# Kernel optimization log

Measured on AMD Instinct MI355X. Metric: run time of the kernel, lower is better.

The kernel has to match this reference:

```python
import jax, jax.numpy as jnp
import numpy as np

NUM_EXPERTS = 8
CAPACITY = 320  # per-batch per-expert token capacity


def setup_inputs() -> dict:
    key = jax.random.key(0)
    k0, k1, k2, k3 = jax.random.split(key, 4)
    B, S, D, F = 4, 2048, 1024, 4096
    E = NUM_EXPERTS
    hidden_states = jax.random.normal(k0, (B, S, D), dtype=jnp.float32)
    gate_w = jax.random.normal(k1, (E, D), dtype=jnp.float32) * 0.02
    w1 = jax.random.normal(k2, (E, D, F), dtype=jnp.float32) * 0.02
    w2 = jax.random.normal(k3, (E, F, D), dtype=jnp.float32) * 0.02
    return {"hidden_states": hidden_states, "gate_w": gate_w, "w1": w1, "w2": w2}


def reference(hidden_states, gate_w, w1, w2):
    E, C = NUM_EXPERTS, CAPACITY
    B, S, D = hidden_states.shape

    # --- route ---
    router_logits = jnp.einsum('bsd,ed->bse', hidden_states, gate_w)
    router_probs = jax.nn.softmax(router_logits, axis=-1)
    expert_idx = jnp.argmax(router_probs, axis=-1)                      # [B,S]
    onehot = jax.nn.one_hot(expert_idx, E, dtype=jnp.int32)             # [B,S,E]
    priority = jnp.cumsum(onehot, axis=1)                               # [B,S,E]
    router_mask = onehot * (priority <= C)                              # [B,S,E]
    assigned = jnp.sum(router_mask, axis=-1) > 0                        # [B,S]
    # slot within expert buffer; dropped tokens go to overflow slot C
    slot = jnp.where(assigned, jnp.sum(priority * onehot, axis=-1) - 1, C)  # [B,S]
    top_prob = jnp.max(router_probs, axis=-1, keepdims=True)            # [B,S,1]

    # --- dispatch: scatter tokens into [B,E,C+1,D] buffers ---
    def dispatch(x_b, e_b, s_b):
        return jnp.zeros((E, C + 1, D), x_b.dtype).at[e_b, s_b].set(x_b)
    buf = jax.vmap(dispatch)(hidden_states, expert_idx, slot)           # [B,E,C+1,D]

    # --- per-expert FFN as grouped GEMM ---
    h = jax.nn.silu(jnp.einsum('becd,edf->becf', buf, w1))
    y = jnp.einsum('becf,efd->becd', h, w2)                             # [B,E,C+1,D]

    # --- combine: gather expert outputs back to token order ---
    gathered = jax.vmap(lambda y_b, e_b, s_b: y_b[e_b, s_b])(y, expert_idx, slot)  # [B,S,D]
    next_states = jnp.where(assigned[..., None], gathered, hidden_states)
    out = top_prob * next_states

    # argmax of capacity-masked one-hot: dropped tokens -> expert 0
    expert_index = jnp.where(assigned, expert_idx, 0)
    return out, router_logits, expert_index
```

## Files before the change

### kernel.cpp

```cpp
#include <hip/hip_runtime.h>

#define B_  4
#define S_  2048
#define D_  1024
#define F_  4096
#define E_  8
#define C_  320
#define CP_ 384
#define NT_ (B_*S_)
#define G_  (B_*E_)

typedef short bf16x8 __attribute__((ext_vector_type(8)));
typedef float f32x4  __attribute__((ext_vector_type(4)));

using gptr_t = const __attribute__((address_space(1))) void*;
using lptr_t = __attribute__((address_space(3))) void*;

__device__ static inline void gll16(const void* g, void* l) {
    __builtin_amdgcn_global_load_lds((gptr_t)g, (lptr_t)l, 16, 0, 0);
}

__device__ static inline unsigned short f2b(float f) {
    unsigned int u = __float_as_uint(f);
    u += 0x7fffu + ((u >> 16) & 1u);
    return (unsigned short)(u >> 16);
}

__global__ __launch_bounds__(256) void k_convT(const float* __restrict__ in,
                                               unsigned short* __restrict__ out,
                                               int R, int Cc) {
    __shared__ unsigned short ld[64][66];
    int e = blockIdx.z;
    const float* src = in + (size_t)e * R * Cc;
    unsigned short* dst = out + (size_t)e * R * Cc;
    int c0 = blockIdx.x * 64, r0 = blockIdx.y * 64;
    int t = threadIdx.x;

    int rr = t >> 4;
    int cg = t & 15;
#pragma unroll
    for (int p = 0; p < 4; p++) {
        int row = p * 16 + rr;
        float4 v = *(const float4*)(src + (size_t)(r0 + row) * Cc + c0 + cg * 4);
        ld[cg * 4 + 0][row] = f2b(v.x);
        ld[cg * 4 + 1][row] = f2b(v.y);
        ld[cg * 4 + 2][row] = f2b(v.z);
        ld[cg * 4 + 3][row] = f2b(v.w);
    }
    __syncthreads();

    int cc = t >> 3;
    int rg = t & 7;
#pragma unroll
    for (int p = 0; p < 2; p++) {
        int col = p * 32 + cc;
        const unsigned* lp = (const unsigned*)&ld[col][rg * 8];
        uint4 w;
        w.x = lp[0]; w.y = lp[1]; w.z = lp[2]; w.w = lp[3];
        *(uint4*)(dst + (size_t)(c0 + col) * R + r0 + rg * 8) = w;
    }
}

__global__ __launch_bounds__(256) void k_router(const float* __restrict__ hs,
                                                const float* __restrict__ gw,
                                                float* __restrict__ logits,
                                                int* __restrict__ eidx,
                                                float* __restrict__ tp) {
    int tok  = (int)((blockIdx.x * 256 + threadIdx.x) >> 6);
    int lane = threadIdx.x & 63;
    const float* x = hs + (size_t)tok * D_;
    double acc[E_];
#pragma unroll
    for (int e = 0; e < E_; e++) acc[e] = 0.0;
    for (int i = 0; i < 16; i++) {
        float xv = x[lane + 64 * i];
#pragma unroll
        for (int e = 0; e < E_; e++)
            acc[e] += (double)xv * (double)gw[e * D_ + lane + 64 * i];
    }
#pragma unroll
    for (int e = 0; e < E_; e++) {
#pragma unroll
        for (int off = 32; off > 0; off >>= 1)
            acc[e] += __shfl_xor(acc[e], off, 64);
    }
    if (lane == 0) {
        float l[E_];
        float mx = -1e30f; int am = 0;
#pragma unroll
        for (int e = 0; e < E_; e++) {
            l[e] = (float)acc[e];
            if (l[e] > mx) { mx = l[e]; am = e; }
        }
        float se = 0.f;
#pragma unroll
        for (int e = 0; e < E_; e++) se += __expf(l[e] - mx);
        tp[tok]   = 1.0f / se;
        eidx[tok] = am;
#pragma unroll
        for (int e = 0; e < E_; e++) logits[(size_t)tok * E_ + e] = l[e];
    }
}

__global__ __launch_bounds__(256) void k_scan(const int* __restrict__ eidx,
                                              int* __restrict__ slot,
                                              int* __restrict__ tok_list,
                                              int* __restrict__ counts,
                                              float* __restrict__ eif) {
    int b = blockIdx.x;
    __shared__ int cCnt[32][E_];
    __shared__ int cBase[32][E_];
    int t = threadIdx.x, wv = t >> 6, lane = t & 63;
    const int* eb = eidx + b * S_;
    for (int c = wv; c < 32; c += 4) {
        int e = eb[c * 64 + lane];
#pragma unroll
        for (int x = 0; x < E_; x++) {
            unsigned long long m = __ballot(e == x);
            if (lane == 0) cCnt[c][x] = __popcll(m);
        }
    }
    __syncthreads();
    if (t < E_) {
        int s = 0;
        for (int c = 0; c < 32; c++) { cBase[c][t] = s; s += cCnt[c][t]; }
        counts[b * E_ + t] = s;
    }
    __syncthreads();
    for (int c = wv; c < 32; c += 4) {
        int s_tok = c * 64 + lane;
        int e = eb[s_tok];
        unsigned long long lowmask = (1ull << lane) - 1ull;
        int rank = 0;
#pragma unroll
        for (int x = 0; x < E_; x++) {
            unsigned long long m = __ballot(e == x);
            if (x == e) rank = __popcll(m & lowmask);
        }
        int pos = cBase[c][e] + rank;
        int assigned = (pos < C_);
        slot[b * S_ + s_tok] = assigned ? pos : C_;
        if (assigned) tok_list[(b * E_ + e) * C_ + pos] = s_tok;
        eif[b * S_ + s_tok] = assigned ? (float)e : 0.0f;
    }
}

__global__ __launch_bounds__(256) void k_dispatch(const float* __restrict__ hs,
                                                  const int* __restrict__ tok_list,
                                                  const int* __restrict__ counts,
                                                  unsigned short* __restrict__ Xd) {
    int w    = (int)((blockIdx.x * 256 + threadIdx.x) >> 6);
    int lane = threadIdx.x & 63;
    int g = w / CP_, row = w % CP_;
    int b = g >> 3;
    int n = min(counts[g], C_);
    unsigned short* drow = Xd + ((size_t)g * CP_ + row) * D_;
    if (row < n) {
        int ts = tok_list[g * C_ + row];
        const float* src = hs + ((size_t)b * S_ + ts) * D_;
#pragma unroll
        for (int i = 0; i < 2; i++) {
            int c0 = (lane + 64 * i) * 8;
            float4 v0 = *(const float4*)(src + c0);
            float4 v1 = *(const float4*)(src + c0 + 4);
            uint4 pk;
            pk.x = (unsigned)f2b(v0.x) | ((unsigned)f2b(v0.y) << 16);
            pk.y = (unsigned)f2b(v0.z) | ((unsigned)f2b(v0.w) << 16);
            pk.z = (unsigned)f2b(v1.x) | ((unsigned)f2b(v1.y) << 16);
            pk.w = (unsigned)f2b(v1.z) | ((unsigned)f2b(v1.w) << 16);
            *(uint4*)(drow + c0) = pk;
        }
    } else {
        uint4 z = {0u, 0u, 0u, 0u};
#pragma unroll
        for (int i = 0; i < 2; i++)
            *(uint4*)(drow + (lane + 64 * i) * 8) = z;
    }
}

__global__ __launch_bounds__(256) void k_ffn1(const unsigned short* __restrict__ Xd,
                                              const unsigned short* __restrict__ w1t,
                                              const int* __restrict__ counts,
                                              unsigned short* __restrict__ h) {
    int zz = blockIdx.z;
    int g = (zz & 3) * 8 + (zz >> 2);
    int n_tok = min(counts[g], C_);
    int m0 = blockIdx.y * 128;
    if (m0 >= n_tok) return;
    int n0 = blockIdx.x * 128;
    int e = g & 7;

    __shared__ unsigned short As[128 * 32];
    __shared__ unsigned short Bs[128 * 32];
    int t = threadIdx.x, lane = t & 63, wv = t >> 6, wm = wv >> 1, wn = wv & 1;

    const unsigned short* Ap = Xd  + (size_t)g * CP_ * D_ + (size_t)(m0 + (t >> 2)) * D_ + (t & 3) * 8;
    const unsigned short* Bp = w1t + (size_t)e * F_ * D_  + (size_t)(n0 + (t >> 2)) * D_ + (t & 3) * 8;

    f32x4 acc[4][4];
    f32x4 z = {0.f, 0.f, 0.f, 0.f};
#pragma unroll
    for (int i = 0; i < 4; i++)
#pragma unroll
        for (int j = 0; j < 4; j++) acc[i][j] = z;

    int ar = (wm * 64 + (lane & 15)) * 32 + (lane >> 4) * 8;
    int br = (wn * 64 + (lane & 15)) * 32 + (lane >> 4) * 8;

    for (int kt = 0; kt < D_; kt += 32) {
        __syncthreads();
        gll16(Ap,            (char*)As + wv * 1024);
        gll16(Ap + 64 * D_,  (char*)As + 4096 + wv * 1024);
        gll16(Bp,            (char*)Bs + wv * 1024);
        gll16(Bp + 64 * D_,  (char*)Bs + 4096 + wv * 1024);
        Ap += 32; Bp += 32;
        __syncthreads();
        bf16x8 a[4], bq[4];
#pragma unroll
        for (int i = 0; i < 4; i++) a[i]  = *(const bf16x8*)&As[ar + i * 512];
#pragma unroll
        for (int j = 0; j < 4; j++) bq[j] = *(const bf16x8*)&Bs[br + j * 512];
#pragma unroll
        for (int i = 0; i < 4; i++)
#pragma unroll
            for (int j = 0; j < 4; j++)
                acc[i][j] = __builtin_amdgcn_mfma_f32_16x16x32_bf16(a[i], bq[j], acc[i][j], 0, 0, 0);
    }

    unsigned short* hb = h + (size_t)g * CP_ * F_;
    int crow = m0 + wm * 64 + (lane >> 4) * 4;
    int ccol = n0 + wn * 64 + (lane & 15);
#pragma unroll
    for (int i = 0; i < 4; i++)
#pragma unroll
        for (int r = 0; r < 4; r++) {
            int row = crow + i * 16 + r;
#pragma unroll
            for (int j = 0; j < 4; j++) {
                float v = acc[i][j][r];
                v = v / (1.0f + __expf(-v));
                hb[(size_t)row * F_ + ccol + j * 16] = f2b(v);
            }
        }
}

__global__ __launch_bounds__(256) void k_ffn2(const unsigned short* __restrict__ h,
                                              const unsigned short* __restrict__ w2t,
                                              const int* __restrict__ counts,
                                              const int* __restrict__ tok_list,
                                              const float* __restrict__ tp,
                                              float* __restrict__ out) {
    int zz = blockIdx.z;
    int g = (zz & 3) * 8 + (zz >> 2);
    int n_tok = min(counts[g], C_);
    int m0 = blockIdx.y * 128;
    if (m0 >= n_tok) return;
    int n0 = blockIdx.x * 128;
    int b = g >> 3, e = g & 7;

    __shared__ unsigned short As[128 * 32];
    __shared__ unsigned short Bs[128 * 32];
    int t = threadIdx.x, lane = t & 63, wv = t >> 6, wm = wv >> 1, wn = wv & 1;

    const unsigned short* Ap = h   + (size_t)g * CP_ * F_ + (size_t)(m0 + (t >> 2)) * F_ + (t & 3) * 8;
    const unsigned short* Bp = w2t + (size_t)e * D_ * F_  + (size_t)(n0 + (t >> 2)) * F_ + (t & 3) * 8;

    f32x4 acc[4][4];
    f32x4 z = {0.f, 0.f, 0.f, 0.f};
#pragma unroll
    for (int i = 0; i < 4; i++)
#pragma unroll
        for (int j = 0; j < 4; j++) acc[i][j] = z;

    int ar = (wm * 64 + (lane & 15)) * 32 + (lane >> 4) * 8;
    int br = (wn * 64 + (lane & 15)) * 32 + (lane >> 4) * 8;

    for (int kt = 0; kt < F_; kt += 32) {
        __syncthreads();
        gll16(Ap,            (char*)As + wv * 1024);
        gll16(Ap + 64 * F_,  (char*)As + 4096 + wv * 1024);
        gll16(Bp,            (char*)Bs + wv * 1024);
        gll16(Bp + 64 * F_,  (char*)Bs + 4096 + wv * 1024);
        Ap += 32; Bp += 32;
        __syncthreads();
        bf16x8 a[4], bq[4];
#pragma unroll
        for (int i = 0; i < 4; i++) a[i]  = *(const bf16x8*)&As[ar + i * 512];
#pragma unroll
        for (int j = 0; j < 4; j++) bq[j] = *(const bf16x8*)&Bs[br + j * 512];
#pragma unroll
        for (int i = 0; i < 4; i++)
#pragma unroll
            for (int j = 0; j < 4; j++)
                acc[i][j] = __builtin_amdgcn_mfma_f32_16x16x32_bf16(a[i], bq[j], acc[i][j], 0, 0, 0);
    }

    int crow = m0 + wm * 64 + (lane >> 4) * 4;
    int ccol = n0 + wn * 64 + (lane & 15);
#pragma unroll
    for (int i = 0; i < 4; i++)
#pragma unroll
        for (int r = 0; r < 4; r++) {
            int row = crow + i * 16 + r;
            if (row < n_tok) {
                int ts = tok_list[g * C_ + row];
                float sc = tp[b * S_ + ts];
                float* orow = out + ((size_t)b * S_ + ts) * D_ + ccol;
#pragma unroll
                for (int j = 0; j < 4; j++)
                    orow[j * 16] = sc * acc[i][j][r];
            }
        }
}

__global__ __launch_bounds__(256) void k_pass(const float* __restrict__ hs,
                                              const int* __restrict__ slot,
                                              const float* __restrict__ tp,
                                              float* __restrict__ out) {
    int tok  = (int)((blockIdx.x * 256 + threadIdx.x) >> 6);
    int lane = threadIdx.x & 63;
    if (slot[tok] < C_) return;
    float sc = tp[tok];
    const float* src = hs + (size_t)tok * D_;
    float* dst = out + (size_t)tok * D_;
#pragma unroll
    for (int i = 0; i < 4; i++) {
        float4 v = *(const float4*)(src + (lane + 64 * i) * 4);
        v.x *= sc; v.y *= sc; v.z *= sc; v.w *= sc;
        *(float4*)(dst + (lane + 64 * i) * 4) = v;
    }
}

extern "C" void kernel_launch(void* const* d_in, const int* in_sizes, int n_in,
                              void* d_out, int out_size, void* d_ws, size_t ws_size,
                              hipStream_t stream) {
    const float* hs = (const float*)d_in[0];
    const float* gw = (const float*)d_in[1];
    const float* w1 = (const float*)d_in[2];
    const float* w2 = (const float*)d_in[3];

    float* out    = (float*)d_out;
    float* logits = out + (size_t)NT_ * D_;
    float* eif    = logits + (size_t)NT_ * E_;

    char* ws = (char*)d_ws;
    int*            eidx     = (int*)(ws + 0);
    int*            slot     = (int*)(ws + 65536);
    float*          tp       = (float*)(ws + 131072);
    int*            tok_list = (int*)(ws + 196608);
    int*            counts   = (int*)(ws + 262144);
    unsigned short* Xd       = (unsigned short*)(ws + 327680);
    unsigned short* w1t      = (unsigned short*)(ws + 33554432ull);
    unsigned short* w2t      = (unsigned short*)(ws + 100663296ull);
    unsigned short* hbuf     = (unsigned short*)(ws + 167772160ull);

    dim3 blk(256);
    k_convT<<<dim3(F_ / 64, D_ / 64, E_), blk, 0, stream>>>(w1, w1t, D_, F_);
    k_convT<<<dim3(D_ / 64, F_ / 64, E_), blk, 0, stream>>>(w2, w2t, F_, D_);
    k_router<<<dim3(NT_ / 4), blk, 0, stream>>>(hs, gw, logits, eidx, tp);
    k_scan<<<dim3(B_), blk, 0, stream>>>(eidx, slot, tok_list, counts, eif);
    k_dispatch<<<dim3(G_ * CP_ / 4), blk, 0, stream>>>(hs, tok_list, counts, Xd);
    k_ffn1<<<dim3(F_ / 128, CP_ / 128, G_), blk, 0, stream>>>(Xd, w1t, counts, hbuf);
    k_ffn2<<<dim3(D_ / 128, CP_ / 128, G_), blk, 0, stream>>>(hbuf, w2t, counts, tok_list, tp, out);
    k_pass<<<dim3(NT_ / 4), blk, 0, stream>>>(hs, slot, tp, out);
}
```

Before: 598.9 us.

## Split-K the second expert GEMM with atomics and swizzle LDS tiles

The second FFN GEMM now splits its K dimension (F) in two, doubling the grid so more blocks run. Each half accumulates into the output with float atomic adds, which requires zeroing the full output buffer with a memset first. Both GEMMs also get an XOR-style column rotation on the global-to-LDS load addresses and the matching fragment reads, meant to cut LDS bank conflicts. The cost is an extra 32 MB memset, atomic traffic, and non-deterministic summation order.

```diff
diff --git a/kernel.cpp b/kernel.cpp
--- a/kernel.cpp
+++ b/kernel.cpp
@@ -178,6 +178,7 @@
     }
 }
 
+
 __global__ __launch_bounds__(256) void k_ffn1(const unsigned short* __restrict__ Xd,
                                               const unsigned short* __restrict__ w1t,
                                               const int* __restrict__ counts,
@@ -194,8 +195,9 @@
     __shared__ unsigned short Bs[128 * 32];
     int t = threadIdx.x, lane = t & 63, wv = t >> 6, wm = wv >> 1, wn = wv & 1;
 
-    const unsigned short* Ap = Xd  + (size_t)g * CP_ * D_ + (size_t)(m0 + (t >> 2)) * D_ + (t & 3) * 8;
-    const unsigned short* Bp = w1t + (size_t)e * F_ * D_  + (size_t)(n0 + (t >> 2)) * D_ + (t & 3) * 8;
+    int cl = ((t & 3) - (t >> 3)) & 3;
+    const unsigned short* Ap = Xd  + (size_t)g * CP_ * D_ + (size_t)(m0 + (t >> 2)) * D_ + cl * 8;
+    const unsigned short* Bp = w1t + (size_t)e * F_ * D_  + (size_t)(n0 + (t >> 2)) * D_ + cl * 8;
 
     f32x4 acc[4][4];
     f32x4 z = {0.f, 0.f, 0.f, 0.f};
@@ -204,8 +206,9 @@
 #pragma unroll
         for (int j = 0; j < 4; j++) acc[i][j] = z;
 
-    int ar = (wm * 64 + (lane & 15)) * 32 + (lane >> 4) * 8;
-    int br = (wn * 64 + (lane & 15)) * 32 + (lane >> 4) * 8;
+    int pc = ((lane >> 4) + ((lane & 15) >> 1)) & 3;
+    int ar = (wm * 64 + (lane & 15)) * 32 + pc * 8;
+    int br = (wn * 64 + (lane & 15)) * 32 + pc * 8;
 
     for (int kt = 0; kt < D_; kt += 32) {
         __syncthreads();
@@ -253,8 +256,9 @@
     int zz = blockIdx.z;
     int g = (zz & 3) * 8 + (zz >> 2);
     int n_tok = min(counts[g], C_);
-    int m0 = blockIdx.y * 128;
+    int m0 = (blockIdx.y >> 1) * 128;
     if (m0 >= n_tok) return;
+    int kp = blockIdx.y & 1;
     int n0 = blockIdx.x * 128;
     int b = g >> 3, e = g & 7;
 
@@ -262,8 +266,9 @@
     __shared__ unsigned short Bs[128 * 32];
     int t = threadIdx.x, lane = t & 63, wv = t >> 6, wm = wv >> 1, wn = wv & 1;
 
-    const unsigned short* Ap = h   + (size_t)g * CP_ * F_ + (size_t)(m0 + (t >> 2)) * F_ + (t & 3) * 8;
-    const unsigned short* Bp = w2t + (size_t)e * D_ * F_  + (size_t)(n0 + (t >> 2)) * F_ + (t & 3) * 8;
+    int cl = ((t & 3) - (t >> 3)) & 3;
+    const unsigned short* Ap = h   + (size_t)g * CP_ * F_ + (size_t)(m0 + (t >> 2)) * F_ + kp * (F_ / 2) + cl * 8;
+    const unsigned short* Bp = w2t + (size_t)e * D_ * F_  + (size_t)(n0 + (t >> 2)) * F_ + kp * (F_ / 2) + cl * 8;
 
     f32x4 acc[4][4];
     f32x4 z = {0.f, 0.f, 0.f, 0.f};
@@ -272,10 +277,11 @@
 #pragma unroll
         for (int j = 0; j < 4; j++) acc[i][j] = z;
 
-    int ar = (wm * 64 + (lane & 15)) * 32 + (lane >> 4) * 8;
-    int br = (wn * 64 + (lane & 15)) * 32 + (lane >> 4) * 8;
-
-    for (int kt = 0; kt < F_; kt += 32) {
+    int pc = ((lane >> 4) + ((lane & 15) >> 1)) & 3;
+    int ar = (wm * 64 + (lane & 15)) * 32 + pc * 8;
+    int br = (wn * 64 + (lane & 15)) * 32 + pc * 8;
+
+    for (int kt = 0; kt < F_ / 2; kt += 32) {
         __syncthreads();
         gll16(Ap,            (char*)As + wv * 1024);
         gll16(Ap + 64 * F_,  (char*)As + 4096 + wv * 1024);
@@ -308,7 +314,7 @@
                 float* orow = out + ((size_t)b * S_ + ts) * D_ + ccol;
 #pragma unroll
                 for (int j = 0; j < 4; j++)
-                    orow[j * 16] = sc * acc[i][j][r];
+                    unsafeAtomicAdd(orow + j * 16, sc * acc[i][j][r]);
             }
         }
 }
@@ -355,12 +361,13 @@
     unsigned short* hbuf     = (unsigned short*)(ws + 167772160ull);
 
     dim3 blk(256);
+    hipMemsetAsync(d_out, 0, (size_t)NT_ * D_ * sizeof(float), stream);
     k_convT<<<dim3(F_ / 64, D_ / 64, E_), blk, 0, stream>>>(w1, w1t, D_, F_);
     k_convT<<<dim3(D_ / 64, F_ / 64, E_), blk, 0, stream>>>(w2, w2t, F_, D_);
     k_router<<<dim3(NT_ / 4), blk, 0, stream>>>(hs, gw, logits, eidx, tp);
     k_scan<<<dim3(B_), blk, 0, stream>>>(eidx, slot, tok_list, counts, eif);
     k_dispatch<<<dim3(G_ * CP_ / 4), blk, 0, stream>>>(hs, tok_list, counts, Xd);
     k_ffn1<<<dim3(F_ / 128, CP_ / 128, G_), blk, 0, stream>>>(Xd, w1t, counts, hbuf);
-    k_ffn2<<<dim3(D_ / 128, CP_ / 128, G_), blk, 0, stream>>>(hbuf, w2t, counts, tok_list, tp, out);
+    k_ffn2<<<dim3(D_ / 128, 2 * CP_ / 128, G_), blk, 0, stream>>>(hbuf, w2t, counts, tok_list, tp, out);
     k_pass<<<dim3(NT_ / 4), blk, 0, stream>>>(hs, slot, tp, out);
 }
```

Result: slower. 637.3 us (+6.4%).
